# Kernel tuning notes

Hardware: AMD Instinct MI355X
Metric: run time of the kernel (lower is better)

The kernel has to match this reference:

```python
import jax, jax.numpy as jnp
import numpy as np
from jax import lax

B, H, W = 4, 256, 256
NF, EMB, IN_NC = 64, 512, 3


def _conv(x, w, b, pad):
    y = lax.conv_general_dilated(x, w, (1, 1), [(pad, pad), (pad, pad)],
                                 dimension_numbers=('NCHW', 'OIHW', 'NCHW'))
    return y + b[None, :, None, None]


def _lrelu(x):
    return jnp.where(x >= 0, x, 0.1 * x)


def _mod_block(x, emb, noise, mw, mb, base_w, cw, cb, wn, k):
    # StyleGAN2_mod: modulate -> demodulate -> groups=B conv -> (+noise) -> 3x3 conv -> lrelu
    b, C, h, w_ = x.shape
    scale = 1.0 / np.sqrt(C * k * k).astype(np.float32)
    style = emb[:, :, 0, 0] @ mw.T + mb                     # [B, C] (1x1 modulation conv)
    wgt = scale * base_w * style[:, None, :, None, None]    # [B, Cout, Cin, k, k]
    demod = lax.rsqrt(jnp.sum(wgt * wgt, axis=(2, 3, 4)) + 1e-8)  # [B, Cout]
    wgt = (wgt * demod[:, :, None, None, None]).reshape(b * C, C, k, k)
    pad = k // 2
    y = lax.conv_general_dilated(x.reshape(1, b * C, h, w_), wgt, (1, 1),
                                 [(pad, pad), (pad, pad)],
                                 dimension_numbers=('NCHW', 'OIHW', 'NCHW'),
                                 feature_group_count=b)
    y = y.reshape(b, C, h, w_)
    if noise is not None:
        y = y + wn * noise                                   # wn init to 0 (as in torch)
    return _lrelu(_conv(y, cw, cb, 1))


def setup_inputs():
    key = jax.random.key(0)
    ks = iter(jax.random.split(key, 64))

    def nrm(shape, s=1.0):
        return s * jax.random.normal(next(ks), shape, dtype=jnp.float32)

    inp = {
        'x': nrm((B, IN_NC, H, W)),
        'embedding': nrm((B, EMB, 1, 1)),
        'noise0': nrm((B, 1, H, W)),
        'noise1': nrm((B, 1, H, W)),
        'noise2': nrm((B, 1, H, W)),
        'w_first': nrm((NF, IN_NC, 3, 3), 0.1), 'b_first': jnp.zeros((NF,), jnp.float32),
        'w_hr1': nrm((NF, NF, 3, 3), 0.05), 'b_hr1': jnp.zeros((NF,), jnp.float32),
        'w_hr2': nrm((NF, NF, 3, 3), 0.05), 'b_hr2': jnp.zeros((NF,), jnp.float32),
        'w_hr3': nrm((NF, NF, 3, 3), 0.05), 'b_hr3': jnp.zeros((NF,), jnp.float32),
        'w_hr4': nrm((NF, NF, 3, 3), 0.05), 'b_hr4': jnp.zeros((NF,), jnp.float32),
        'w_hr5': nrm((NF, NF, 3, 3), 0.05), 'b_hr5': jnp.zeros((NF,), jnp.float32),
        'w_last': nrm((3, NF, 3, 3), 0.05), 'b_last': jnp.zeros((3,), jnp.float32),
    }
    for i in range(3):
        inp[f'mod{i}_mw'] = nrm((NF, EMB), 0.05)       # 1x1 modulation conv weight
        inp[f'mod{i}_mb'] = jnp.ones((NF,), jnp.float32)
        inp[f'mod{i}_w'] = nrm((1, NF, NF, 3, 3))      # torch.randn init
        inp[f'mod{i}_cw'] = nrm((NF, NF, 3, 3), 0.05)  # conv_last of mod block
        inp[f'mod{i}_cb'] = jnp.zeros((NF,), jnp.float32)
        inp[f'mod{i}_wn'] = jnp.zeros((), jnp.float32)  # weight_noise param (init 0)
    return inp


def reference(x, embedding, noise0, noise1, noise2,
              w_first, b_first, w_hr1, b_hr1, w_hr2, b_hr2, w_hr3, b_hr3,
              w_hr4, b_hr4, w_hr5, b_hr5, w_last, b_last,
              mod0_mw, mod0_mb, mod0_w, mod0_cw, mod0_cb, mod0_wn,
              mod1_mw, mod1_mb, mod1_w, mod1_cw, mod1_cb, mod1_wn,
              mod2_mw, mod2_mb, mod2_w, mod2_cw, mod2_cb, mod2_wn):
    out = _lrelu(_conv(x, w_first, b_first, 1))
    out = _mod_block(out, embedding, noise0, mod0_mw, mod0_mb, mod0_w, mod0_cw, mod0_cb, mod0_wn, 3)
    out = _conv(out, w_hr1, b_hr1, 1)
    out = _mod_block(out, embedding, noise1, mod1_mw, mod1_mb, mod1_w, mod1_cw, mod1_cb, mod1_wn, 3)
    out = _conv(out, w_hr2, b_hr2, 1)
    out = _mod_block(out, embedding, noise2, mod2_mw, mod2_mb, mod2_w, mod2_cw, mod2_cb, mod2_wn, 3)
    out = _conv(out, w_hr3, b_hr3, 1)
    # modulation3/4/5 results are discarded in the original forward (dead code);
    # they do not affect the output, so they are omitted here.
    out = _conv(out, w_hr4, b_hr4, 1)
    out = _conv(out, w_hr5, b_hr5, 1)
    out = _conv(out, w_last, b_last, 1)
    return out
```

## Files before the change

### kernel.cpp

```cpp
#include <hip/hip_runtime.h>
#include <cstddef>

#define HH 256
#define WW 256
#define NB 4
#define NFC 64
#define EMBC 512

typedef short s16x8 __attribute__((ext_vector_type(8)));
typedef float f32x4 __attribute__((ext_vector_type(4)));

#define GLOBAL_AS __attribute__((address_space(1)))
#define LDS_AS __attribute__((address_space(3)))

static __device__ __forceinline__ unsigned short f2b(float f) {
    unsigned int u = __float_as_uint(f);
    u += 0x7FFFu + ((u >> 16) & 1u);
    return (unsigned short)(u >> 16);
}

__global__ void modw3_kernel(
    const float* __restrict__ emb,
    const float* __restrict__ mw0, const float* __restrict__ mb0, const float* __restrict__ bw0,
    const float* __restrict__ mw1, const float* __restrict__ mb1, const float* __restrict__ bw1,
    const float* __restrict__ mw2, const float* __restrict__ mb2, const float* __restrict__ bw2,
    unsigned short* __restrict__ outw, size_t ostride)
{
    const int co = blockIdx.x, b = blockIdx.y;
    const int ci = threadIdx.x;
    const float *mw, *mb, *bw;
    switch (blockIdx.z) {
        case 0:  mw = mw0; mb = mb0; bw = bw0; break;
        case 1:  mw = mw1; mb = mb1; bw = bw1; break;
        default: mw = mw2; mb = mb2; bw = bw2; break;
    }

    const float* e = emb + (size_t)b * EMBC;
    const float* m = mw + (size_t)ci * EMBC;
    float s = mb[ci];
    for (int k = 0; k < EMBC; k += 4) {
        float4 ev = *(const float4*)(e + k);
        float4 mv = *(const float4*)(m + k);
        s += ev.x * mv.x + ev.y * mv.y + ev.z * mv.z + ev.w * mv.w;
    }

    float w[9];
    float ss = 0.f;
    const float* src = bw + ((size_t)co * NFC + ci) * 9;
#pragma unroll
    for (int k = 0; k < 9; ++k) {
        float v = (1.0f / 24.0f) * src[k] * s;
        w[k] = v;
        ss += v * v;
    }
#pragma unroll
    for (int off = 32; off; off >>= 1) ss += __shfl_xor(ss, off);
    float demod = rsqrtf(ss + 1e-8f);

    unsigned short* o = outw + (size_t)blockIdx.z * ostride;
#pragma unroll
    for (int k = 0; k < 9; ++k)
        o[(((size_t)b * 9 + k) * NFC + co) * NFC + ci] = f2b(w[k] * demod);
}

__global__ void fixw8_kernel(
    const float* __restrict__ w0, const float* __restrict__ w1,
    const float* __restrict__ w2, const float* __restrict__ w3,
    const float* __restrict__ w4, const float* __restrict__ w5,
    const float* __restrict__ w6, const float* __restrict__ w7,
    unsigned short* __restrict__ wt)
{
    const int idx = blockIdx.x * 256 + threadIdx.x;
    const float* w;
    switch (blockIdx.y) {
        case 0: w = w0; break;  case 1: w = w1; break;
        case 2: w = w2; break;  case 3: w = w3; break;
        case 4: w = w4; break;  case 5: w = w5; break;
        case 6: w = w6; break;  default: w = w7; break;
    }
    const int k = idx / (NFC * NFC);
    const int rem = idx - k * (NFC * NFC);
    const int co = rem / NFC, ci = rem - co * NFC;
    wt[(size_t)blockIdx.y * 9 * NFC * NFC + idx] = f2b(w[((size_t)co * NFC + ci) * 9 + k]);
}

__global__ void fixw_last_kernel(const float* __restrict__ w, unsigned short* __restrict__ wt)
{
    int idx = blockIdx.x * 256 + threadIdx.x;
    if (idx >= 9 * 16 * NFC) return;
    int k = idx / (16 * NFC);
    int rem = idx - k * (16 * NFC);
    int co = rem / NFC, ci = rem - co * NFC;
    float v = (co < 3) ? w[((size_t)co * NFC + ci) * 9 + k] : 0.f;
    wt[idx] = f2b(v);
}

__global__ void firstw_kernel(const float* __restrict__ w, unsigned short* __restrict__ wt)
{
    int idx = blockIdx.x * 256 + threadIdx.x;
    if (idx >= 64 * 32) return;
    int co = idx >> 5, k = idx & 31;
    wt[idx] = (k < 27) ? f2b(w[co * 27 + k]) : 0;
}

__global__ __launch_bounds__(256) void conv_first_fused(
    const float* __restrict__ x, const unsigned short* __restrict__ wt,
    const float* __restrict__ bias, unsigned short* __restrict__ out)
{
    __shared__ float xf[3][18][20];
    __shared__ unsigned short col[256][36];

    const int tid = threadIdx.x;
    const int flat = blockIdx.x;
    const int swz = (flat & 7) * 128 + (flat >> 3);
    const int b = swz >> 8, remb = swz & 255;
    const int h0 = (remb >> 4) * 16, w0 = (remb & 15) * 16;

    const int lane = tid & 63, wid = tid >> 6;
    const int m16 = lane & 15, kg = lane >> 4;

    s16x8 a[4];
    float4 bv[4];
#pragma unroll
    for (int mf = 0; mf < 4; ++mf) {
        a[mf] = *(const s16x8*)(wt + (mf * 16 + m16) * 32 + kg * 8);
        bv[mf] = *(const float4*)(bias + mf * 16 + kg * 4);
    }

#pragma unroll 1
    for (int idx = tid; idx < 972; idx += 256) {
        const int ci = idx / 324, rem2 = idx - ci * 324;
        const int row = rem2 / 18, colw = rem2 - row * 18;
        const int gh = h0 + row - 1, gw = w0 + colw - 1;
        float v = 0.f;
        if ((unsigned)gh < HH && (unsigned)gw < WW)
            v = x[(((size_t)b * 3 + ci) * HH + gh) * WW + gw];
        xf[ci][row][colw] = v;
    }
    __syncthreads();

    {
        const int h = tid >> 4, w = tid & 15;
        unsigned short kv[32];
#pragma unroll
        for (int ci = 0; ci < 3; ++ci)
#pragma unroll
            for (int kh = 0; kh < 3; ++kh)
#pragma unroll
                for (int kw = 0; kw < 3; ++kw)
                    kv[ci * 9 + kh * 3 + kw] = f2b(xf[ci][h + kh][w + kw]);
#pragma unroll
        for (int k = 27; k < 32; ++k) kv[k] = 0;
#pragma unroll
        for (int q = 0; q < 4; ++q)
            *(uint4*)&col[tid][q * 8] = *(const uint4*)(kv + q * 8);
    }
    __syncthreads();

#pragma unroll
    for (int t = 0; t < 4; ++t) {
        const int p = wid * 64 + t * 16 + m16;
        s16x8 bfr = *(const s16x8*)&col[p][kg * 8];
#pragma unroll
        for (int mf = 0; mf < 4; ++mf) {
            f32x4 c = (f32x4)(0.f);
            c = __builtin_amdgcn_mfma_f32_16x16x32_bf16(a[mf], bfr, c, 0, 0, 0);
            unsigned short pk[4];
#pragma unroll
            for (int e = 0; e < 4; ++e) {
                float v = c[e] + (&bv[mf].x)[e];
                v = v >= 0.f ? v : 0.1f * v;
                pk[e] = f2b(v);
            }
            const int h = h0 + (p >> 4), w = w0 + (p & 15);
            *(ushort4*)(out + (((size_t)b * HH + h) * WW + w) * NFC + mf * 16 + kg * 4)
                = *(ushort4*)pk;
        }
    }
}

template <int MFRAGS, bool PERB, bool BIAS, bool LRELU, bool NOISE, bool OUTF32>
__global__ __launch_bounds__(512, 1) void mconv(
    const unsigned short* __restrict__ in, const unsigned short* __restrict__ wt,
    const float* __restrict__ bias, const float* __restrict__ noise,
    const float* __restrict__ wnp, void* __restrict__ outv)
{
    constexpr int COP = MFRAGS * 16;
    constexpr int WELEM = 9 * COP * NFC;
    constexpr int NWDMA = WELEM * 2 / 1024;
    __shared__ unsigned short wl[WELEM];
    __shared__ uint4 xs[2][18 * 18 * 8];

    const int tid = threadIdx.x;
    const int lane = tid & 63, wid = tid >> 6;
    const int m16 = lane & 15, kg = lane >> 4;

    const int hw = blockIdx.x;
    const int n = (hw & 7) * 32 + (hw >> 3);
    const int b = n >> 6;

    const unsigned short* wsrc = PERB ? wt + (size_t)b * WELEM : wt;
    for (int i = wid; i < NWDMA; i += 8) {
        const unsigned short* gp = wsrc + i * 512 + (lane >> 3) * 64
                                   + (((lane & 7) ^ (lane >> 3)) << 3);
        __builtin_amdgcn_global_load_lds(
            (const GLOBAL_AS void*)gp, (LDS_AS void*)(wl + i * 512), 16, 0, 0);
    }

    auto stage_tile = [&](int tt, uint4* buf) {
        const int remb = tt & 255;
        const int th = remb >> 4, tw = remb & 15;
        const int h0 = th * 16, w0 = tw * 16;
        const bool interior = (th > 0) && (th < 15) && (tw > 0) && (tw < 15);
        if (interior) {
            for (int i = wid; i < 54; i += 8) {
                const int row = i / 3, part = i - row * 3;
                const int j0 = (part == 0) ? -1 : (part == 1) ? 7 : 9;
                const int gh = h0 + row - 1;
                const int j = j0 + (lane >> 3);
                const int gw = w0 + j;
                const int w = j + 1;
                const unsigned short* gp = in + (((size_t)b * HH + gh) * WW + gw) * NFC
                                              + ((lane & 7) ^ (w & 7)) * 8;
                uint4* lp = buf + (size_t)(row * 18 + (j0 + 1)) * 8;
                __builtin_amdgcn_global_load_lds(
                    (const GLOBAL_AS void*)gp, (LDS_AS void*)lp, 16, 0, 0);
            }
        } else {
#pragma unroll 1
            for (int idx = tid; idx < 2592; idx += 512) {
                const int row = idx / 144, rem2 = idx - row * 144;
                const int w = rem2 >> 3, slot = rem2 & 7;
                const int gh = h0 + row - 1, gw = w0 + w - 1;
                uint4 u = make_uint4(0, 0, 0, 0);
                if ((unsigned)gh < HH && (unsigned)gw < WW)
                    u = *(const uint4*)(in + (((size_t)b * HH + gh) * WW + gw) * NFC + slot * 8);
                buf[(row * 18 + w) * 8 + (slot ^ (w & 7))] = u;
            }
        }
    };

    stage_tile(n * 4, xs[0]);
    __syncthreads();

    const float wn = NOISE ? wnp[0] : 0.f;

#pragma unroll 1
    for (int k = 0; k < 4; ++k) {
        const int tt = n * 4 + k;
        const int remb = tt & 255;
        const int h0 = (remb >> 4) * 16, w0 = (remb & 15) * 16;
        const uint4* buf = xs[k & 1];

        if (k < 3) stage_tile(tt + 1, xs[(k + 1) & 1]);

        f32x4 acc[MFRAGS][2];
#pragma unroll
        for (int mf = 0; mf < MFRAGS; ++mf)
#pragma unroll
            for (int r = 0; r < 2; ++r) acc[mf][r] = (f32x4)(0.f);

        s16x8 abuf[2][MFRAGS];
        s16x8 bbuf[2][2];

        auto LOADG = [&](int g, int par) {
            const int tap = g >> 1, half = g & 1;
            const int kh = tap / 3, kw = tap - kh * 3;
            const int lw = m16 + kw;
            const int slot = (half * 4 + kg) ^ (lw & 7);
#pragma unroll
            for (int mf = 0; mf < MFRAGS; ++mf) {
                const int eoff = (tap * COP + mf * 16 + m16) * NFC
                                 + (((half * 4 + kg) * 8) ^ ((m16 & 7) << 3));
                abuf[par][mf] = *(const s16x8*)(wl + eoff);
            }
#pragma unroll
            for (int r = 0; r < 2; ++r) {
                const int lrow = wid * 2 + r + kh;
                bbuf[par][r] = *(const s16x8*)&buf[(lrow * 18 + lw) * 8 + slot];
            }
        };

        LOADG(0, 0);
#pragma unroll
        for (int g = 0; g < 18; ++g) {
            if (g + 1 < 18) LOADG(g + 1, (g + 1) & 1);
#pragma unroll
            for (int r = 0; r < 2; ++r)
#pragma unroll
                for (int mf = 0; mf < MFRAGS; ++mf)
                    acc[mf][r] = __builtin_amdgcn_mfma_f32_16x16x32_bf16(
                        abuf[g & 1][mf], bbuf[g & 1][r], acc[mf][r], 0, 0, 0);
        }

        const int wcol = w0 + m16;
#pragma unroll
        for (int r = 0; r < 2; ++r) {
            const int h = h0 + wid * 2 + r;
            float nz = 0.f;
            if (NOISE) nz = noise[((size_t)b * HH + h) * WW + wcol];
#pragma unroll
            for (int mf = 0; mf < MFRAGS; ++mf) {
                const int cob = mf * 16 + kg * 4;
                f32x4 v = acc[mf][r];
                float4 bvv = make_float4(0.f, 0.f, 0.f, 0.f);
                if (BIAS) bvv = *(const float4*)(bias + cob);
                float o[4];
#pragma unroll
                for (int e = 0; e < 4; ++e) {
                    float t = v[e] + (BIAS ? (&bvv.x)[e] : 0.f);
                    if (NOISE) t += wn * nz;
                    if (LRELU) t = t >= 0.f ? t : 0.1f * t;
                    o[e] = t;
                }
                if (OUTF32) {
                    float* of = (float*)outv;
#pragma unroll
                    for (int e = 0; e < 4; ++e) {
                        int co = cob + e;
                        if (co < 3)
                            of[(((size_t)b * 3 + co) * HH + h) * WW + wcol] = o[e];
                    }
                } else {
                    unsigned short pk[4];
#pragma unroll
                    for (int e = 0; e < 4; ++e) pk[e] = f2b(o[e]);
                    unsigned short* ob = (unsigned short*)outv;
                    *(ushort4*)(ob + (((size_t)b * HH + h) * WW + wcol) * NFC + cob) = *(ushort4*)pk;
                }
            }
        }
        __syncthreads();
    }
}

extern "C" void kernel_launch(void* const* d_in, const int* in_sizes, int n_in,
                              void* d_out, int out_size, void* d_ws, size_t ws_size,
                              hipStream_t stream)
{
    auto F = [&](int i) { return (const float*)d_in[i]; };
    const float* x       = F(0);
    const float* emb     = F(1);
    const float* noise[3] = {F(2), F(3), F(4)};
    const float* w_first = F(5);  const float* b_first = F(6);
    const float* w_hr[5] = {F(7), F(9), F(11), F(13), F(15)};
    const float* b_hr[5] = {F(8), F(10), F(12), F(14), F(16)};
    const float* w_last  = F(17); const float* b_last = F(18);
    const float *m_mw[3], *m_mb[3], *m_w[3], *m_cw[3], *m_cb[3], *m_wn[3];
    for (int i = 0; i < 3; ++i) {
        int o = 19 + 6 * i;
        m_mw[i] = F(o); m_mb[i] = F(o + 1); m_w[i] = F(o + 2);
        m_cw[i] = F(o + 3); m_cb[i] = F(o + 4); m_wn[i] = F(o + 5);
    }

    const size_t ACT  = (size_t)NB * HH * WW * NFC;
    const size_t MODW = (size_t)NB * 9 * NFC * NFC;
    const size_t FIXW = (size_t)9 * NFC * NFC;
    unsigned short* act0 = (unsigned short*)d_ws;
    unsigned short* act1 = act0 + ACT;
    unsigned short* wmod = act1 + ACT;
    unsigned short* wfix = wmod + 3 * MODW;
    unsigned short* wlast = wfix + 8 * FIXW;
    unsigned short* wfirst = wlast + 9 * 16 * NFC;

    modw3_kernel<<<dim3(NFC, NB, 3), NFC, 0, stream>>>(
        emb, m_mw[0], m_mb[0], m_w[0], m_mw[1], m_mb[1], m_w[1],
        m_mw[2], m_mb[2], m_w[2], wmod, MODW);
    fixw8_kernel<<<dim3(144, 8), 256, 0, stream>>>(
        m_cw[0], m_cw[1], m_cw[2], w_hr[0], w_hr[1], w_hr[2], w_hr[3], w_hr[4], wfix);
    fixw_last_kernel<<<(9 * 16 * 64 + 255) / 256, 256, 0, stream>>>(w_last, wlast);
    firstw_kernel<<<8, 256, 0, stream>>>(w_first, wfirst);

    conv_first_fused<<<1024, 256, 0, stream>>>(x, wfirst, b_first, act0);

    const int grid = 256;
    unsigned short* cur = act0;
    unsigned short* nxt = act1;
    auto swap = [&]() { unsigned short* t = cur; cur = nxt; nxt = t; };

    for (int i = 0; i < 3; ++i) {
        mconv<4, true, false, false, true, false>
            <<<grid, 512, 0, stream>>>(cur, wmod + i * MODW, nullptr, noise[i], m_wn[i], nxt);
        swap();
        mconv<4, false, true, true, false, false>
            <<<grid, 512, 0, stream>>>(cur, wfix + i * FIXW, m_cb[i], nullptr, nullptr, nxt);
        swap();
        mconv<4, false, true, false, false, false>
            <<<grid, 512, 0, stream>>>(cur, wfix + (3 + i) * FIXW, b_hr[i], nullptr, nullptr, nxt);
        swap();
    }
    mconv<4, false, true, false, false, false>
        <<<grid, 512, 0, stream>>>(cur, wfix + 6 * FIXW, b_hr[3], nullptr, nullptr, nxt);
    swap();
    mconv<4, false, true, false, false, false>
        <<<grid, 512, 0, stream>>>(cur, wfix + 7 * FIXW, b_hr[4], nullptr, nullptr, nxt);
    swap();
    mconv<1, false, true, false, false, true>
        <<<grid, 512, 0, stream>>>(cur, wlast, b_last, nullptr, nullptr, d_out);
}
```

Before: 354.6 us.

## Hold conv weights in registers and split waves by output-channel group

Each wave now loads its share of the 3x3 conv weights straight from global memory into registers once per block, instead of staging all weights in LDS and re-reading them for every MFMA step. Waves are split into output-channel groups (2 groups of 32 channels) that each cover 4 rows, so per-step LDS traffic drops to activation fragments only. The cost is much higher VGPR use (36 weight fragments per lane) and redundant global weight reads across blocks, which rely on cache hits.

```diff
diff --git a/kernel.cpp b/kernel.cpp
--- a/kernel.cpp
+++ b/kernel.cpp
@@ -179,32 +179,37 @@
     }
 }
 
-template <int MFRAGS, bool PERB, bool BIAS, bool LRELU, bool NOISE, bool OUTF32>
+template <int MFW, int NCOG, bool PERB, bool BIAS, bool LRELU, bool NOISE, bool OUTF32>
 __global__ __launch_bounds__(512, 1) void mconv(
     const unsigned short* __restrict__ in, const unsigned short* __restrict__ wt,
     const float* __restrict__ bias, const float* __restrict__ noise,
     const float* __restrict__ wnp, void* __restrict__ outv)
 {
-    constexpr int COP = MFRAGS * 16;
+    constexpr int COP = MFW * 16 * NCOG;
+    constexpr int RPW = 16 / (8 / NCOG);
     constexpr int WELEM = 9 * COP * NFC;
-    constexpr int NWDMA = WELEM * 2 / 1024;
-    __shared__ unsigned short wl[WELEM];
     __shared__ uint4 xs[2][18 * 18 * 8];
 
     const int tid = threadIdx.x;
     const int lane = tid & 63, wid = tid >> 6;
     const int m16 = lane & 15, kg = lane >> 4;
+    const int cog = wid % NCOG;
+    const int rg = wid / NCOG;
 
     const int hw = blockIdx.x;
     const int n = (hw & 7) * 32 + (hw >> 3);
     const int b = n >> 6;
 
     const unsigned short* wsrc = PERB ? wt + (size_t)b * WELEM : wt;
-    for (int i = wid; i < NWDMA; i += 8) {
-        const unsigned short* gp = wsrc + i * 512 + (lane >> 3) * 64
-                                   + (((lane & 7) ^ (lane >> 3)) << 3);
-        __builtin_amdgcn_global_load_lds(
-            (const GLOBAL_AS void*)gp, (LDS_AS void*)(wl + i * 512), 16, 0, 0);
+    s16x8 a_regs[18][MFW];
+#pragma unroll
+    for (int g = 0; g < 18; ++g) {
+        const int tap = g >> 1, half = g & 1;
+#pragma unroll
+        for (int mf = 0; mf < MFW; ++mf)
+            a_regs[g][mf] = *(const s16x8*)(wsrc
+                + ((size_t)tap * COP + cog * MFW * 16 + mf * 16 + m16) * NFC
+                + half * 32 + kg * 8);
     }
 
     auto stage_tile = [&](int tt, uint4* buf) {
@@ -254,54 +259,46 @@
 
         if (k < 3) stage_tile(tt + 1, xs[(k + 1) & 1]);
 
-        f32x4 acc[MFRAGS][2];
-#pragma unroll
-        for (int mf = 0; mf < MFRAGS; ++mf)
-#pragma unroll
-            for (int r = 0; r < 2; ++r) acc[mf][r] = (f32x4)(0.f);
-
-        s16x8 abuf[2][MFRAGS];
-        s16x8 bbuf[2][2];
-
-        auto LOADG = [&](int g, int par) {
+        f32x4 acc[MFW][RPW];
+#pragma unroll
+        for (int mf = 0; mf < MFW; ++mf)
+#pragma unroll
+            for (int r = 0; r < RPW; ++r) acc[mf][r] = (f32x4)(0.f);
+
+        s16x8 bbuf[2][RPW];
+        auto LOADB = [&](int g, int par) {
             const int tap = g >> 1, half = g & 1;
             const int kh = tap / 3, kw = tap - kh * 3;
             const int lw = m16 + kw;
             const int slot = (half * 4 + kg) ^ (lw & 7);
 #pragma unroll
-            for (int mf = 0; mf < MFRAGS; ++mf) {
-                const int eoff = (tap * COP + mf * 16 + m16) * NFC
-                                 + (((half * 4 + kg) * 8) ^ ((m16 & 7) << 3));
-                abuf[par][mf] = *(const s16x8*)(wl + eoff);
-            }
-#pragma unroll
-            for (int r = 0; r < 2; ++r) {
-                const int lrow = wid * 2 + r + kh;
+            for (int r = 0; r < RPW; ++r) {
+                const int lrow = rg * RPW + r + kh;
                 bbuf[par][r] = *(const s16x8*)&buf[(lrow * 18 + lw) * 8 + slot];
             }
         };
 
-        LOADG(0, 0);
+        LOADB(0, 0);
 #pragma unroll
         for (int g = 0; g < 18; ++g) {
-            if (g + 1 < 18) LOADG(g + 1, (g + 1) & 1);
-#pragma unroll
-            for (int r = 0; r < 2; ++r)
-#pragma unroll
-                for (int mf = 0; mf < MFRAGS; ++mf)
+            if (g + 1 < 18) LOADB(g + 1, (g + 1) & 1);
+#pragma unroll
+            for (int r = 0; r < RPW; ++r)
+#pragma unroll
+                for (int mf = 0; mf < MFW; ++mf)
                     acc[mf][r] = __builtin_amdgcn_mfma_f32_16x16x32_bf16(
-                        abuf[g & 1][mf], bbuf[g & 1][r], acc[mf][r], 0, 0, 0);
+                        a_regs[g][mf], bbuf[g & 1][r], acc[mf][r], 0, 0, 0);
         }
 
         const int wcol = w0 + m16;
 #pragma unroll
-        for (int r = 0; r < 2; ++r) {
-            const int h = h0 + wid * 2 + r;
+        for (int r = 0; r < RPW; ++r) {
+            const int h = h0 + rg * RPW + r;
             float nz = 0.f;
             if (NOISE) nz = noise[((size_t)b * HH + h) * WW + wcol];
 #pragma unroll
-            for (int mf = 0; mf < MFRAGS; ++mf) {
-                const int cob = mf * 16 + kg * 4;
+            for (int mf = 0; mf < MFW; ++mf) {
+                const int cob = cog * MFW * 16 + mf * 16 + kg * 4;
                 f32x4 v = acc[mf][r];
                 float4 bvv = make_float4(0.f, 0.f, 0.f, 0.f);
                 if (BIAS) bvv = *(const float4*)(bias + cob);
@@ -379,22 +376,22 @@
     auto swap = [&]() { unsigned short* t = cur; cur = nxt; nxt = t; };
 
     for (int i = 0; i < 3; ++i) {
-        mconv<4, true, false, false, true, false>
+        mconv<2, 2, true, false, false, true, false>
             <<<grid, 512, 0, stream>>>(cur, wmod + i * MODW, nullptr, noise[i], m_wn[i], nxt);
         swap();
-        mconv<4, false, true, true, false, false>
+        mconv<2, 2, false, true, true, false, false>
             <<<grid, 512, 0, stream>>>(cur, wfix + i * FIXW, m_cb[i], nullptr, nullptr, nxt);
         swap();
-        mconv<4, false, true, false, false, false>
+        mconv<2, 2, false, true, false, false, false>
             <<<grid, 512, 0, stream>>>(cur, wfix + (3 + i) * FIXW, b_hr[i], nullptr, nullptr, nxt);
         swap();
     }
-    mconv<4, false, true, false, false, false>
+    mconv<2, 2, false, true, false, false, false>
         <<<grid, 512, 0, stream>>>(cur, wfix + 6 * FIXW, b_hr[3], nullptr, nullptr, nxt);
     swap();
-    mconv<4, false, true, false, false, false>
+    mconv<2, 2, false, true, false, false, false>
         <<<grid, 512, 0, stream>>>(cur, wfix + 7 * FIXW, b_hr[4], nullptr, nullptr, nxt);
     swap();
-    mconv<1, false, true, false, false, true>
+    mconv<1, 1, false, true, false, false, true>
         <<<grid, 512, 0, stream>>>(cur, wlast, b_last, nullptr, nullptr, d_out);
 }
```

Result: slower. 499.0 us (+40.7%).
